# Optimization experiments

Hardware: AMD Instinct MI355X
Metric: run time of the kernel (lower is better)

## Reference

```python
import jax, jax.numpy as jnp
import numpy as np

D_MODEL = 1024
N_HEADS = 16
D_K = D_MODEL // N_HEADS
SCALE = float(np.sqrt(D_K))


def setup_inputs() -> dict:
    key = jax.random.key(0)
    ks = jax.random.split(key, 11)
    B, L, D = 2, 2048, D_MODEL
    s = 1.0 / np.sqrt(D)
    inp = {
        "q": jax.random.normal(ks[0], (B, L, D), dtype=jnp.float32),
        "k": jax.random.normal(ks[1], (B, L, D), dtype=jnp.float32),
        "v": jax.random.normal(ks[2], (B, L, D), dtype=jnp.float32),
        "Wq": jax.random.normal(ks[3], (D, D), dtype=jnp.float32) * s,
        "bq": jnp.zeros((D,), dtype=jnp.float32),
        "Wk": jax.random.normal(ks[4], (D, D), dtype=jnp.float32) * s,
        "bk": jnp.zeros((D,), dtype=jnp.float32),
        "Wv": jax.random.normal(ks[5], (D, D), dtype=jnp.float32) * s,
        "bv": jnp.zeros((D,), dtype=jnp.float32),
        "Wo": jax.random.normal(ks[6], (D, D), dtype=jnp.float32) * s,
        "bo": jnp.zeros((D,), dtype=jnp.float32),
    }
    return inp


def reference(q, k, v, Wq, bq, Wk, bk, Wv, bv, Wo, bo):
    B, L, D = q.shape
    H, Dk = N_HEADS, D_K
    # projections: [B,L,D] -> [B,H,L,Dk]
    def proj(x, W, b):
        y = x @ W + b
        return y.reshape(B, -1, H, Dk).transpose(0, 2, 1, 3)
    qh = proj(q, Wq, bq)
    kh = proj(k, Wk, bk)
    vh = proj(v, Wv, bv)
    # scores [B,H,Lq,Lk]
    scores = jnp.einsum("bhqd,bhkd->bhqk", qh, kh) / SCALE
    attn = jax.nn.softmax(scores, axis=-1)  # dropout=0.0 -> identity
    out = jnp.einsum("bhqk,bhkd->bhqd", attn, vh)
    out = out.transpose(0, 2, 1, 3).reshape(B, -1, D)
    return out @ Wo + bo
```

## Files before the change

kernel.cpp:

```cpp
#include <hip/hip_runtime.h>
#include <hip/hip_bf16.h>
#include <stdint.h>
#include <stddef.h>

typedef unsigned short ushortT;
typedef __attribute__((ext_vector_type(8))) short bf16x8s;
typedef __attribute__((ext_vector_type(4))) float f32x4;


__device__ __forceinline__ short f2bf(float f) {
  unsigned u = __float_as_uint(f);
  u += 0x7FFFu + ((u >> 16) & 1u);
  return (short)(u >> 16);
}

__device__ __forceinline__ bf16x8s cvt8(const float* src) {
  const float4* p = (const float4*)src;
  float4 a = p[0], b = p[1];
  bf16x8s r;
  r[0] = f2bf(a.x); r[1] = f2bf(a.y); r[2] = f2bf(a.z); r[3] = f2bf(a.w);
  r[4] = f2bf(b.x); r[5] = f2bf(b.y); r[6] = f2bf(b.z); r[7] = f2bf(b.w);
  return r;
}

__device__ __forceinline__ void load_lds16(const ushortT* g, ushortT* l) {
  __builtin_amdgcn_global_load_lds(
      (const __attribute__((address_space(1))) void*)(g),
      (__attribute__((address_space(3))) void*)(l), 16, 0, 0);
}

__global__ __launch_bounds__(256)
void prep(const float* __restrict__ q, const float* __restrict__ k,
          const float* __restrict__ v,
          const float* __restrict__ Wq, const float* __restrict__ Wk,
          const float* __restrict__ Wv, const float* __restrict__ Wo,
          ushortT* __restrict__ Qc, ushortT* __restrict__ Kc,
          ushortT* __restrict__ Vc, ushortT* __restrict__ Wt)
{
  const int z = blockIdx.z;
  if (z < 4) {
    if (blockIdx.x >= 1024) return;
    __shared__ __align__(16) ushortT t[32][33];
    const float* W = (z == 0) ? Wq : (z == 1) ? Wk : (z == 2) ? Wv : Wo;
    ushortT* dst = Wt + (size_t)z * 1024 * 1024;
    const int x = (blockIdx.x & 31) * 32, y = (blockIdx.x >> 5) * 32;
    const int tx = threadIdx.x & 31, ty = threadIdx.x >> 5;
#pragma unroll
    for (int i = ty; i < 32; i += 8)
      t[i][tx] = (ushortT)f2bf(W[(size_t)(y + i) * 1024 + x + tx]);
    __syncthreads();
#pragma unroll
    for (int i = ty; i < 32; i += 8)
      dst[(size_t)(x + i) * 1024 + y + tx] = t[tx][i];
  } else {
    const float* src = (z == 4) ? q : (z == 5) ? k : v;
    ushortT* dst = (z == 4) ? Qc : (z == 5) ? Kc : Vc;
    const size_t i8 = ((size_t)blockIdx.x * 256 + threadIdx.x) * 8;
    *(bf16x8s*)(dst + i8) = cvt8(src + i8);
  }
}

__device__ __forceinline__ void gemm_core_128(
    const ushortT* __restrict__ A, const ushortT* __restrict__ Bt,
    int K, ushortT* As, ushortT* Bs, f32x4 (&acc)[4][4], int m0, int n0)
{
  const int tid  = threadIdx.x;
  const int wave = tid >> 6, lane = tid & 63;
  const int wm = (wave & 1) << 6;
  const int wn = (wave >> 1) << 6;
  const int lr = lane & 15;
  const int lk = (lane >> 4) << 3;

#pragma unroll
  for (int mi = 0; mi < 4; ++mi)
#pragma unroll
    for (int ni = 0; ni < 4; ++ni)
      acc[mi][ni] = (f32x4){0.f, 0.f, 0.f, 0.f};

  for (int k0 = 0; k0 < K; k0 += 32) {
    __syncthreads();
#pragma unroll
    for (int i = 0; i < 2; ++i) {
      const int cc  = tid + (i << 8);
      const int row = cc >> 2;
      const int ko  = (cc & 3) << 3;
      load_lds16(A  + (size_t)(m0 + row) * K + k0 + ko, As + cc * 8);
      load_lds16(Bt + (size_t)(n0 + row) * K + k0 + ko, Bs + cc * 8);
    }
    __syncthreads();

    bf16x8s af[4], bfr[4];
#pragma unroll
    for (int i = 0; i < 4; ++i)
      af[i] = *(const bf16x8s*)(As + (wm + i * 16 + lr) * 32 + lk);
#pragma unroll
    for (int i = 0; i < 4; ++i)
      bfr[i] = *(const bf16x8s*)(Bs + (wn + i * 16 + lr) * 32 + lk);

#pragma unroll
    for (int mi = 0; mi < 4; ++mi)
#pragma unroll
      for (int ni = 0; ni < 4; ++ni)
        acc[mi][ni] = __builtin_amdgcn_mfma_f32_16x16x32_bf16(
            af[mi], bfr[ni], acc[mi][ni], 0, 0, 0);
  }
}

__global__ __launch_bounds__(256)
void proj_gemm(const ushortT* __restrict__ Qc, const ushortT* __restrict__ Kc,
               const ushortT* __restrict__ Vc, const ushortT* __restrict__ WtAll,
               const float* __restrict__ bq, const float* __restrict__ bk,
               const float* __restrict__ bv,
               ushortT* __restrict__ Qh, ushortT* __restrict__ Kh,
               ushortT* __restrict__ Vt)
{
  __shared__ __align__(16) ushortT As[128 * 32];
  __shared__ __align__(16) ushortT Bs[128 * 32];
  const int which = blockIdx.z;
  const ushortT* A  = (which == 0) ? Qc : (which == 1) ? Kc : Vc;
  const ushortT* Bt = WtAll + (size_t)which * 1024 * 1024;
  const float* bias = (which == 0) ? bq : (which == 1) ? bk : bv;
  const int m0 = blockIdx.x * 128, n0 = blockIdx.y * 128;

  f32x4 acc[4][4];
  gemm_core_128(A, Bt, 1024, As, Bs, acc, m0, n0);

  const int lane = threadIdx.x & 63, wave = threadIdx.x >> 6;
  const int wm = (wave & 1) << 6, wn = (wave >> 1) << 6;
  const int lr = lane & 15, quad = lane >> 4;
  const float QSCALE = 0.18033688011112042f;

#pragma unroll
  for (int ni = 0; ni < 4; ++ni) {
    const int n = n0 + wn + ni * 16 + lr;
    const float bias_v = bias[n];
    const int h = n >> 6, d = n & 63;
#pragma unroll
    for (int mi = 0; mi < 4; ++mi) {
#pragma unroll
      for (int r = 0; r < 4; ++r) {
        const int m = m0 + wm + mi * 16 + quad * 4 + r;
        const int b = m >> 11, l = m & 2047;
        float val = acc[mi][ni][r] + bias_v;
        if (which == 0) val *= QSCALE;
        const ushortT o = (ushortT)f2bf(val);
        const size_t bh = (size_t)(b * 16 + h);
        if (which == 0)      Qh[(bh * 2048 + l) * 64 + d] = o;
        else if (which == 1) Kh[(bh * 2048 + l) * 64 + d] = o;
        else                 Vt[(bh * 64 + d) * 2048 + l] = o;
      }
    }
  }
}

__global__ __launch_bounds__(256)
void attn_kernel(const ushortT* __restrict__ Qh, const ushortT* __restrict__ Kh,
                 const ushortT* __restrict__ Vt, ushortT* __restrict__ Ob)
{
  const int b = blockIdx.z, h = blockIdx.y, qt = blockIdx.x;
  const int bh = b * 16 + h;
  const int wave = threadIdx.x >> 6, lane = threadIdx.x & 63;
  const int lr = lane & 15, quad = lane >> 4, lk = quad * 8;
  const int q0 = qt * 128 + wave * 32;

  const ushortT* Q = Qh + ((size_t)bh * 2048 + q0) * 64;
  const ushortT* K = Kh + (size_t)bh * 2048 * 64;
  const ushortT* V = Vt + (size_t)bh * 64 * 2048;

  __shared__ __align__(16) ushortT Ks[64 * 76];
  __shared__ __align__(16) ushortT Vs[64 * 76];
  __shared__ __align__(16) ushortT P4[4][32 * 88];
  ushortT* Pw = P4[wave];

  bf16x8s qf[2][2];
#pragma unroll
  for (int mt = 0; mt < 2; ++mt) {
    qf[mt][0] = *(const bf16x8s*)(Q + (mt * 16 + lr) * 64 + lk);
    qf[mt][1] = *(const bf16x8s*)(Q + (mt * 16 + lr) * 64 + 32 + lk);
  }

  f32x4 o[2][4];
#pragma unroll
  for (int mt = 0; mt < 2; ++mt)
#pragma unroll
    for (int nt = 0; nt < 4; ++nt) o[mt][nt] = (f32x4){0.f, 0.f, 0.f, 0.f};
  float lsum[2] = {0.f, 0.f};

  const int tid = threadIdx.x;
  const int srow = tid >> 3;
  const int sc8  = (tid & 7) << 3;

  for (int kt = 0; kt < 2048; kt += 64) {
    bf16x8s kch[2], vch[2];
#pragma unroll
    for (int i = 0; i < 2; ++i) {
      const int row = srow + i * 32;
      kch[i] = *(const bf16x8s*)(K + (size_t)(kt + row) * 64 + sc8);
      vch[i] = *(const bf16x8s*)(V + (size_t)row * 2048 + kt + sc8);
    }
    __syncthreads();
#pragma unroll
    for (int i = 0; i < 2; ++i) {
      const int row = srow + i * 32;
      *(bf16x8s*)(Ks + row * 76 + sc8) = kch[i];
      *(bf16x8s*)(Vs + row * 76 + sc8) = vch[i];
    }
    __syncthreads();

    f32x4 s[2][4];
#pragma unroll
    for (int mt = 0; mt < 2; ++mt)
#pragma unroll
      for (int t = 0; t < 4; ++t) s[mt][t] = (f32x4){0.f, 0.f, 0.f, 0.f};
#pragma unroll
    for (int t = 0; t < 4; ++t) {
      const bf16x8s kf0 = *(const bf16x8s*)(Ks + (t * 16 + lr) * 76 + lk);
      const bf16x8s kf1 = *(const bf16x8s*)(Ks + (t * 16 + lr) * 76 + 32 + lk);
#pragma unroll
      for (int mt = 0; mt < 2; ++mt) {
        s[mt][t] = __builtin_amdgcn_mfma_f32_16x16x32_bf16(kf0, qf[mt][0], s[mt][t], 0, 0, 0);
        s[mt][t] = __builtin_amdgcn_mfma_f32_16x16x32_bf16(kf1, qf[mt][1], s[mt][t], 0, 0, 0);
      }
    }

#pragma unroll
    for (int mt = 0; mt < 2; ++mt)
#pragma unroll
      for (int t = 0; t < 4; ++t) {
        const float e0 = __builtin_amdgcn_exp2f(s[mt][t][0]);
        const float e1 = __builtin_amdgcn_exp2f(s[mt][t][1]);
        const float e2 = __builtin_amdgcn_exp2f(s[mt][t][2]);
        const float e3 = __builtin_amdgcn_exp2f(s[mt][t][3]);
        lsum[mt] += (e0 + e1) + (e2 + e3);
        const unsigned a0 = __float_as_uint(e0) + 0x8000u;
        const unsigned a1 = __float_as_uint(e1) + 0x8000u;
        const unsigned a2 = __float_as_uint(e2) + 0x8000u;
        const unsigned a3 = __float_as_uint(e3) + 0x8000u;
        uint2 d;
        d.x = (a0 >> 16) | (a1 & 0xFFFF0000u);
        d.y = (a2 >> 16) | (a3 & 0xFFFF0000u);
        *(uint2*)(Pw + (mt * 16 + lr) * 88 + t * 16 + quad * 4) = d;
      }
    asm volatile("s_waitcnt lgkmcnt(0)" ::: "memory");

    bf16x8s pf[2][2];
#pragma unroll
    for (int mt = 0; mt < 2; ++mt) {
      pf[mt][0] = *(const bf16x8s*)(Pw + (mt * 16 + lr) * 88 + lk);
      pf[mt][1] = *(const bf16x8s*)(Pw + (mt * 16 + lr) * 88 + 32 + lk);
    }
#pragma unroll
    for (int nt = 0; nt < 4; ++nt) {
      const bf16x8s vf0 = *(const bf16x8s*)(Vs + (nt * 16 + lr) * 76 + lk);
      const bf16x8s vf1 = *(const bf16x8s*)(Vs + (nt * 16 + lr) * 76 + 32 + lk);
#pragma unroll
      for (int mt = 0; mt < 2; ++mt) {
        o[mt][nt] = __builtin_amdgcn_mfma_f32_16x16x32_bf16(pf[mt][0], vf0, o[mt][nt], 0, 0, 0);
        o[mt][nt] = __builtin_amdgcn_mfma_f32_16x16x32_bf16(pf[mt][1], vf1, o[mt][nt], 0, 0, 0);
      }
    }
  }

  float* fP = (float*)Pw;
#pragma unroll
  for (int mt = 0; mt < 2; ++mt) {
    float s = lsum[mt];
    s += __shfl_xor(s, 16);
    s += __shfl_xor(s, 32);
    fP[mt * 16 + lr] = 1.0f / s;
  }
  asm volatile("s_waitcnt lgkmcnt(0)" ::: "memory");
  float invr[2][4];
#pragma unroll
  for (int mt = 0; mt < 2; ++mt)
#pragma unroll
    for (int r = 0; r < 4; ++r) invr[mt][r] = fP[mt * 16 + quad * 4 + r];

#pragma unroll
  for (int mt = 0; mt < 2; ++mt)
#pragma unroll
    for (int nt = 0; nt < 4; ++nt) {
      const int dcol = h * 64 + nt * 16 + lr;
#pragma unroll
      for (int r = 0; r < 4; ++r) {
        const int l = q0 + mt * 16 + quad * 4 + r;
        Ob[((size_t)b * 2048 + l) * 1024 + dcol] =
            (ushortT)f2bf(o[mt][nt][r] * invr[mt][r]);
      }
    }
}

__global__ __launch_bounds__(256)
void out_gemm(const ushortT* __restrict__ Ob, const ushortT* __restrict__ Wto,
              const float* __restrict__ bo, float* __restrict__ C)
{
  __shared__ __align__(16) ushortT As[128 * 32];
  __shared__ __align__(16) ushortT Bs[128 * 32];
  const int m0 = blockIdx.x * 128, n0 = blockIdx.y * 128;

  f32x4 acc[4][4];
  gemm_core_128(Ob, Wto, 1024, As, Bs, acc, m0, n0);

  const int lane = threadIdx.x & 63, wave = threadIdx.x >> 6;
  const int wm = (wave & 1) << 6, wn = (wave >> 1) << 6;
  const int lr = lane & 15, quad = lane >> 4;

#pragma unroll
  for (int ni = 0; ni < 4; ++ni) {
    const int n = n0 + wn + ni * 16 + lr;
    const float bias_v = bo[n];
#pragma unroll
    for (int mi = 0; mi < 4; ++mi) {
#pragma unroll
      for (int r = 0; r < 4; ++r) {
        const int m = m0 + wm + mi * 16 + quad * 4 + r;
        C[(size_t)m * 1024 + n] = acc[mi][ni][r] + bias_v;
      }
    }
  }
}

extern "C" void kernel_launch(void* const* d_in, const int* in_sizes, int n_in,
                              void* d_out, int out_size, void* d_ws, size_t ws_size,
                              hipStream_t stream) {
  const float* q  = (const float*)d_in[0];
  const float* k  = (const float*)d_in[1];
  const float* v  = (const float*)d_in[2];
  const float* Wq = (const float*)d_in[3];
  const float* bq = (const float*)d_in[4];
  const float* Wk = (const float*)d_in[5];
  const float* bk = (const float*)d_in[6];
  const float* Wv = (const float*)d_in[7];
  const float* bv = (const float*)d_in[8];
  const float* Wo = (const float*)d_in[9];
  const float* bo = (const float*)d_in[10];

  char* ws = (char*)d_ws;
  ushortT* Wt = (ushortT*)(ws);
  ushortT* Qh = (ushortT*)(ws + (size_t)(8  << 20));
  ushortT* Kh = (ushortT*)(ws + (size_t)(16 << 20));
  ushortT* Vt = (ushortT*)(ws + (size_t)(24 << 20));
  ushortT* Qc = (ushortT*)(ws + (size_t)(32 << 20));
  ushortT* Kc = (ushortT*)(ws + (size_t)(40 << 20));
  ushortT* Vc = (ushortT*)(ws + (size_t)(48 << 20));
  ushortT* Ob = Qc;

  prep<<<dim3(2048, 1, 7), 256, 0, stream>>>(q, k, v, Wq, Wk, Wv, Wo,
                                             Qc, Kc, Vc, Wt);
  proj_gemm<<<dim3(32, 8, 3), 256, 0, stream>>>(Qc, Kc, Vc, Wt, bq, bk, bv,
                                                Qh, Kh, Vt);
  attn_kernel<<<dim3(16, 16, 2), 256, 0, stream>>>(Qh, Kh, Vt, Ob);
  out_gemm<<<dim3(32, 8), 256, 0, stream>>>(Ob, Wt + (size_t)3 * 1024 * 1024,
                                            bo, (float*)d_out);
}
```

Measured before the change: 239.1 us.

## Prefetch K/V tiles, use packed bf16 convert, set MFMA priority, retile out GEMM

The attention loop now issues the global loads for the next K/V tile right after the LDS stores, so their latency overlaps the current tile's MFMA and softmax work. Softmax probabilities are packed to bf16 with a single v_cvt_pk_bf16_f32 instruction, and the P scratch row stride shrinks from 88 to 84. s_setprio is raised around the MFMA blocks. The output GEMM uses 128x64 tiles via direct global-to-LDS loads, doubling the block count to fill more CUs. The price is extra registers for the prefetch buffers, one wasted wrap-around load on the final iteration, and a possible change in LDS bank conflicts from the new P stride.

```diff
diff --git a/kernel.cpp b/kernel.cpp
--- a/kernel.cpp
+++ b/kernel.cpp
@@ -20,6 +20,12 @@
   bf16x8s r;
   r[0] = f2bf(a.x); r[1] = f2bf(a.y); r[2] = f2bf(a.z); r[3] = f2bf(a.w);
   r[4] = f2bf(b.x); r[5] = f2bf(b.y); r[6] = f2bf(b.z); r[7] = f2bf(b.w);
+  return r;
+}
+
+__device__ __forceinline__ unsigned cvtpk_bf16(float lo, float hi) {
+  unsigned r;
+  asm("v_cvt_pk_bf16_f32 %0, %1, %2" : "=v"(r) : "v"(lo), "v"(hi));
   return r;
 }
 
@@ -169,7 +175,7 @@
 
   __shared__ __align__(16) ushortT Ks[64 * 76];
   __shared__ __align__(16) ushortT Vs[64 * 76];
-  __shared__ __align__(16) ushortT P4[4][32 * 88];
+  __shared__ __align__(16) ushortT P4[4][32 * 84];
   ushortT* Pw = P4[wave];
 
   bf16x8s qf[2][2];
@@ -189,66 +195,71 @@
   const int tid = threadIdx.x;
   const int srow = tid >> 3;
   const int sc8  = (tid & 7) << 3;
+  const ushortT* Kg = K + (size_t)srow * 64 + sc8;
+  const ushortT* Vg = V + (size_t)srow * 2048 + sc8;
+
+  bf16x8s kch[2], vch[2];
+  kch[0] = *(const bf16x8s*)(Kg);
+  kch[1] = *(const bf16x8s*)(Kg + 32 * 64);
+  vch[0] = *(const bf16x8s*)(Vg);
+  vch[1] = *(const bf16x8s*)(Vg + 32 * 2048);
 
   for (int kt = 0; kt < 2048; kt += 64) {
-    bf16x8s kch[2], vch[2];
-#pragma unroll
-    for (int i = 0; i < 2; ++i) {
-      const int row = srow + i * 32;
-      kch[i] = *(const bf16x8s*)(K + (size_t)(kt + row) * 64 + sc8);
-      vch[i] = *(const bf16x8s*)(V + (size_t)row * 2048 + kt + sc8);
-    }
-    __syncthreads();
-#pragma unroll
-    for (int i = 0; i < 2; ++i) {
-      const int row = srow + i * 32;
-      *(bf16x8s*)(Ks + row * 76 + sc8) = kch[i];
-      *(bf16x8s*)(Vs + row * 76 + sc8) = vch[i];
-    }
-    __syncthreads();
-
-    f32x4 s[2][4];
+    __syncthreads();
+    *(bf16x8s*)(Ks + srow * 76 + sc8)        = kch[0];
+    *(bf16x8s*)(Ks + (srow + 32) * 76 + sc8) = kch[1];
+    *(bf16x8s*)(Vs + srow * 76 + sc8)        = vch[0];
+    *(bf16x8s*)(Vs + (srow + 32) * 76 + sc8) = vch[1];
+    __syncthreads();
+
+    const int ktn = (kt + 64) & 2047;
+    kch[0] = *(const bf16x8s*)(Kg + (size_t)ktn * 64);
+    kch[1] = *(const bf16x8s*)(Kg + (size_t)(ktn + 32) * 64);
+    vch[0] = *(const bf16x8s*)(Vg + ktn);
+    vch[1] = *(const bf16x8s*)(Vg + 32 * 2048 + ktn);
+
+    f32x4 s4[2][4];
 #pragma unroll
     for (int mt = 0; mt < 2; ++mt)
 #pragma unroll
-      for (int t = 0; t < 4; ++t) s[mt][t] = (f32x4){0.f, 0.f, 0.f, 0.f};
+      for (int t = 0; t < 4; ++t) s4[mt][t] = (f32x4){0.f, 0.f, 0.f, 0.f};
+
+    __builtin_amdgcn_s_setprio(1);
 #pragma unroll
     for (int t = 0; t < 4; ++t) {
       const bf16x8s kf0 = *(const bf16x8s*)(Ks + (t * 16 + lr) * 76 + lk);
       const bf16x8s kf1 = *(const bf16x8s*)(Ks + (t * 16 + lr) * 76 + 32 + lk);
 #pragma unroll
       for (int mt = 0; mt < 2; ++mt) {
-        s[mt][t] = __builtin_amdgcn_mfma_f32_16x16x32_bf16(kf0, qf[mt][0], s[mt][t], 0, 0, 0);
-        s[mt][t] = __builtin_amdgcn_mfma_f32_16x16x32_bf16(kf1, qf[mt][1], s[mt][t], 0, 0, 0);
-      }
-    }
+        s4[mt][t] = __builtin_amdgcn_mfma_f32_16x16x32_bf16(kf0, qf[mt][0], s4[mt][t], 0, 0, 0);
+        s4[mt][t] = __builtin_amdgcn_mfma_f32_16x16x32_bf16(kf1, qf[mt][1], s4[mt][t], 0, 0, 0);
+      }
+    }
+    __builtin_amdgcn_s_setprio(0);
 
 #pragma unroll
     for (int mt = 0; mt < 2; ++mt)
 #pragma unroll
       for (int t = 0; t < 4; ++t) {
-        const float e0 = __builtin_amdgcn_exp2f(s[mt][t][0]);
-        const float e1 = __builtin_amdgcn_exp2f(s[mt][t][1]);
-        const float e2 = __builtin_amdgcn_exp2f(s[mt][t][2]);
-        const float e3 = __builtin_amdgcn_exp2f(s[mt][t][3]);
+        const float e0 = __builtin_amdgcn_exp2f(s4[mt][t][0]);
+        const float e1 = __builtin_amdgcn_exp2f(s4[mt][t][1]);
+        const float e2 = __builtin_amdgcn_exp2f(s4[mt][t][2]);
+        const float e3 = __builtin_amdgcn_exp2f(s4[mt][t][3]);
         lsum[mt] += (e0 + e1) + (e2 + e3);
-        const unsigned a0 = __float_as_uint(e0) + 0x8000u;
-        const unsigned a1 = __float_as_uint(e1) + 0x8000u;
-        const unsigned a2 = __float_as_uint(e2) + 0x8000u;
-        const unsigned a3 = __float_as_uint(e3) + 0x8000u;
         uint2 d;
-        d.x = (a0 >> 16) | (a1 & 0xFFFF0000u);
-        d.y = (a2 >> 16) | (a3 & 0xFFFF0000u);
-        *(uint2*)(Pw + (mt * 16 + lr) * 88 + t * 16 + quad * 4) = d;
+        d.x = cvtpk_bf16(e0, e1);
+        d.y = cvtpk_bf16(e2, e3);
+        *(uint2*)(Pw + (mt * 16 + lr) * 84 + t * 16 + quad * 4) = d;
       }
     asm volatile("s_waitcnt lgkmcnt(0)" ::: "memory");
 
     bf16x8s pf[2][2];
 #pragma unroll
     for (int mt = 0; mt < 2; ++mt) {
-      pf[mt][0] = *(const bf16x8s*)(Pw + (mt * 16 + lr) * 88 + lk);
-      pf[mt][1] = *(const bf16x8s*)(Pw + (mt * 16 + lr) * 88 + 32 + lk);
-    }
+      pf[mt][0] = *(const bf16x8s*)(Pw + (mt * 16 + lr) * 84 + lk);
+      pf[mt][1] = *(const bf16x8s*)(Pw + (mt * 16 + lr) * 84 + 32 + lk);
+    }
+    __builtin_amdgcn_s_setprio(1);
 #pragma unroll
     for (int nt = 0; nt < 4; ++nt) {
       const bf16x8s vf0 = *(const bf16x8s*)(Vs + (nt * 16 + lr) * 76 + lk);
@@ -259,6 +270,7 @@
         o[mt][nt] = __builtin_amdgcn_mfma_f32_16x16x32_bf16(pf[mt][1], vf1, o[mt][nt], 0, 0, 0);
       }
     }
+    __builtin_amdgcn_s_setprio(0);
   }
 
   float* fP = (float*)Pw;
@@ -295,18 +307,48 @@
               const float* __restrict__ bo, float* __restrict__ C)
 {
   __shared__ __align__(16) ushortT As[128 * 32];
-  __shared__ __align__(16) ushortT Bs[128 * 32];
-  const int m0 = blockIdx.x * 128, n0 = blockIdx.y * 128;
-
-  f32x4 acc[4][4];
-  gemm_core_128(Ob, Wto, 1024, As, Bs, acc, m0, n0);
-
-  const int lane = threadIdx.x & 63, wave = threadIdx.x >> 6;
-  const int wm = (wave & 1) << 6, wn = (wave >> 1) << 6;
-  const int lr = lane & 15, quad = lane >> 4;
-
-#pragma unroll
-  for (int ni = 0; ni < 4; ++ni) {
+  __shared__ __align__(16) ushortT Bs[64 * 32];
+  const int m0 = blockIdx.x * 128, n0 = blockIdx.y * 64;
+  const int tid = threadIdx.x;
+  const int wave = tid >> 6, lane = tid & 63;
+  const int wm = (wave & 1) << 6;
+  const int wn = (wave >> 1) << 5;
+  const int lr = lane & 15, lk = (lane >> 4) << 3;
+
+  f32x4 acc[4][2];
+#pragma unroll
+  for (int mi = 0; mi < 4; ++mi)
+#pragma unroll
+    for (int ni = 0; ni < 2; ++ni) acc[mi][ni] = (f32x4){0.f, 0.f, 0.f, 0.f};
+
+  const int row = tid >> 2;
+  const int ko  = (tid & 3) << 3;
+  for (int k0 = 0; k0 < 1024; k0 += 32) {
+    __syncthreads();
+    load_lds16(Ob  + (size_t)(m0 + row) * 1024 + k0 + ko,      As + row * 32 + ko);
+    load_lds16(Ob  + (size_t)(m0 + 64 + row) * 1024 + k0 + ko, As + (64 + row) * 32 + ko);
+    load_lds16(Wto + (size_t)(n0 + row) * 1024 + k0 + ko,      Bs + row * 32 + ko);
+    __syncthreads();
+
+    bf16x8s af[4], bfr[2];
+#pragma unroll
+    for (int i = 0; i < 4; ++i)
+      af[i] = *(const bf16x8s*)(As + (wm + i * 16 + lr) * 32 + lk);
+#pragma unroll
+    for (int i = 0; i < 2; ++i)
+      bfr[i] = *(const bf16x8s*)(Bs + (wn + i * 16 + lr) * 32 + lk);
+
+#pragma unroll
+    for (int mi = 0; mi < 4; ++mi)
+#pragma unroll
+      for (int ni = 0; ni < 2; ++ni)
+        acc[mi][ni] = __builtin_amdgcn_mfma_f32_16x16x32_bf16(
+            af[mi], bfr[ni], acc[mi][ni], 0, 0, 0);
+  }
+
+  const int quad = lane >> 4;
+#pragma unroll
+  for (int ni = 0; ni < 2; ++ni) {
     const int n = n0 + wn + ni * 16 + lr;
     const float bias_v = bo[n];
 #pragma unroll
@@ -350,6 +392,6 @@
   proj_gemm<<<dim3(32, 8, 3), 256, 0, stream>>>(Qc, Kc, Vc, Wt, bq, bk, bv,
                                                 Qh, Kh, Vt);
   attn_kernel<<<dim3(16, 16, 2), 256, 0, stream>>>(Qh, Kh, Vt, Ob);
-  out_gemm<<<dim3(32, 8), 256, 0, stream>>>(Ob, Wt + (size_t)3 * 1024 * 1024,
-                                            bo, (float*)d_out);
-}
+  out_gemm<<<dim3(32, 16), 256, 0, stream>>>(Ob, Wt + (size_t)3 * 1024 * 1024,
+                                             bo, (float*)d_out);
+}
```

Result: slower. 252.3 us (+5.5%).
